# Kernel tuning notes

Measured on AMD Instinct MI355X. Metric: run time of the kernel, lower is better.

The kernel has to match this reference:

```python
import jax, jax.numpy as jnp
import numpy as np

B, S, D = 4, 2048, 512
BETA = 1.0
PARAM_SCALE = 1.0 / np.sqrt(D)  # ~ torch Linear default init scale


def setup_inputs() -> dict:
    key = jax.random.key(0)
    ks = jax.random.split(key, 14)
    def rn(k, shape, scale=1.0):
        return (jax.random.normal(k, shape, jnp.float32) * scale).astype(jnp.float32)
    return {
        "x_re": rn(ks[0], (B, S, D)),
        "x_im": rn(ks[1], (B, S, D)),
        "Wq_re": rn(ks[2], (D, D), PARAM_SCALE), "Wq_im": rn(ks[3], (D, D), PARAM_SCALE),
        "bq_re": rn(ks[4], (D,), PARAM_SCALE),   "bq_im": rn(ks[5], (D,), PARAM_SCALE),
        "Wk_re": rn(ks[6], (D, D), PARAM_SCALE), "Wk_im": rn(ks[7], (D, D), PARAM_SCALE),
        "bk_re": rn(ks[8], (D,), PARAM_SCALE),   "bk_im": rn(ks[9], (D,), PARAM_SCALE),
        "Wv_re": rn(ks[10], (D, D), PARAM_SCALE), "Wv_im": rn(ks[11], (D, D), PARAM_SCALE),
        "bv_re": rn(ks[12], (D,), PARAM_SCALE),   "bv_im": rn(ks[13], (D,), PARAM_SCALE),
    }


def reference(x_re, x_im, Wq_re, Wq_im, bq_re, bq_im,
              Wk_re, Wk_im, bk_re, bk_im, Wv_re, Wv_im, bv_re, bv_im):
    cx = lambda re, im: (re + 1j * im).astype(jnp.complex64)
    x = cx(x_re, x_im)                          # [B,S,D] complex64
    # nn.Linear: y = x @ W.T + b (complex)
    Q = jnp.einsum('bsd,ed->bse', x, cx(Wq_re, Wq_im)) + cx(bq_re, bq_im)
    K = jnp.einsum('bsd,ed->bse', x, cx(Wk_re, Wk_im)) + cx(bk_re, bk_im)
    V = jnp.einsum('bsd,ed->bse', x, cx(Wv_re, Wv_im)) + cx(bv_re, bv_im)
    # energy = -Re(Q K^H); attn = softmax(-beta * energy) = softmax(beta * Re(Q K^H))
    scores = jnp.real(jnp.einsum('bse,bte->bst', Q, jnp.conj(K)))  # [B,S,S] float32
    attn = jax.nn.softmax(BETA * scores, axis=-1)
    out = jnp.einsum('bst,bte->bse', attn.astype(jnp.complex64), V)  # [B,S,D] complex64
    return out
```

## Files before the change

### kernel.cpp

```cpp
#include <hip/hip_runtime.h>
#include <hip/hip_bf16.h>
#include <cstdint>
#include <cstddef>


typedef unsigned short u16;
typedef __attribute__((ext_vector_type(8))) _Float16 half8;
typedef __attribute__((ext_vector_type(4))) float f32x4;

#define B_    4
#define S_    2048
#define D_    512
#define M_TOT (B_ * S_)
#define KC    (2 * D_)
#define N1    (6 * D_)
#define RE_PLANE 4194304

#define X_ELEMS  ((size_t)M_TOT * KC)
#define W_ELEMS  ((size_t)N1 * KC)
#define QK_ELEMS ((size_t)M_TOT * KC)
#define VT_ELEMS ((size_t)B_ * KC * S_)
#define AT_ELEMS ((size_t)M_TOT * S_)

__device__ __forceinline__ u16 f2h(float f) {
    _Float16 h = (_Float16)f;
    return __builtin_bit_cast(u16, h);
}
__device__ __forceinline__ float h2f(u16 b) {
    return (float)__builtin_bit_cast(_Float16, b);
}

__device__ __forceinline__ f32x4 mfma16(half8 a, half8 b, f32x4 c) {
    return __builtin_amdgcn_mfma_f32_16x16x32_f16(a, b, c, 0, 0, 0);
}

__device__ __forceinline__ void dma16(const u16* g, u16* l) {
    __builtin_amdgcn_global_load_lds(
        (const __attribute__((address_space(1))) unsigned int*)g,
        (__attribute__((address_space(3))) unsigned int*)l,
        16, 0, 0);
}

__device__ __forceinline__ void stage_half(u16* __restrict__ plane,
                                           const u16* __restrict__ src,
                                           int rowbase, int kcol, int tid) {
#pragma unroll
    for (int i = 0; i < 2; ++i) {
        int c = tid + (i << 9);
        int c2 = c ^ (((c >> 5) & 1) << 1);
        int row = ((c2 >> 3) << 1) | ((c2 >> 2) & 1);
        int ks = c2 & 3;
        dma16(src + (size_t)(rowbase + row) * KC + (kcol + ks * 8),
              plane + c * 8);
    }
}

__device__ __forceinline__ void stage_half8(u16* __restrict__ plane,
                                            const u16* __restrict__ src,
                                            int ld, int rowbase, int kcol,
                                            int tid) {
#pragma unroll
    for (int i = 0; i < 2; ++i) {
        int c = tid + (i << 8);
        int c2 = c ^ (((c >> 5) & 1) << 1);
        int row = ((c2 >> 3) << 1) | ((c2 >> 2) & 1);
        int ks = c2 & 3;
        dma16(src + (size_t)(rowbase + row) * ld + (kcol + ks * 8),
              plane + c * 8);
    }
}

#define VMW(N) asm volatile("s_waitcnt vmcnt(" #N ")" ::: "memory")
#define BAR()  __builtin_amdgcn_s_barrier()

__global__ void k_diag(float* __restrict__ out, int out_size, float val) {
    int i = blockIdx.x * 256 + threadIdx.x;
    if (i < out_size && i < 4096) out[i] = val;
}

__global__ void k_prep(const float* __restrict__ xr, const float* __restrict__ xi,
                       const float* __restrict__ Wqr, const float* __restrict__ Wqi,
                       const float* __restrict__ Wkr, const float* __restrict__ Wki,
                       const float* __restrict__ Wvr, const float* __restrict__ Wvi,
                       const float* __restrict__ bqr, const float* __restrict__ bqi,
                       const float* __restrict__ bkr, const float* __restrict__ bki,
                       const float* __restrict__ bvr, const float* __restrict__ bvi,
                       u16* __restrict__ Xh, u16* __restrict__ Xl,
                       u16* __restrict__ Wh, float* __restrict__ bc) {
    int gb = blockIdx.x;
    int tid = threadIdx.x;
    if (gb < 16384) {
        int id = gb * 256 + tid;
        int m = id >> 9, d = id & 511;
        size_t o = (size_t)m * KC + d;
        if (o + D_ >= X_ELEMS) return;
        float vr = xr[id], vi = xi[id];
        u16 h;
        h = f2h(vr); Xh[o] = h;        Xl[o] = f2h(vr - h2f(h));
        h = f2h(vi); Xh[o + D_] = h;   Xl[o + D_] = f2h(vi - h2f(h));
    } else if (gb < 16384 + 12288) {
        int id = (gb - 16384) * 256 + tid;
        int n = id >> 10, k = id & 1023;
        int q = n >> 9, e = n & 511;
        int half = k >> 9, d = k & 511;
        const float* Wre = (q < 2) ? Wqr : ((q < 4) ? Wkr : Wvr);
        const float* Wim = (q < 2) ? Wqi : ((q < 4) ? Wki : Wvi);
        size_t src = (size_t)e * D_ + d;
        float v;
        if ((q & 1) == 0) v = half ? -Wim[src] : Wre[src];
        else              v = half ?  Wre[src] : Wim[src];
        if ((size_t)id < W_ELEMS) Wh[id] = f2h(v);
    } else {
        int id = (gb - 16384 - 12288) * 256 + tid;
        if (id >= N1) return;
        int q = id >> 9, e = id & 511;
        const float* src = (q == 0) ? bqr : (q == 1) ? bqi : (q == 2) ? bkr
                         : (q == 3) ? bki : (q == 4) ? bvr : bvi;
        bc[id] = src[e];
    }
}

#define RDA(d, pl, mg)                                                        \
  { const u16* _pa = &lds[pl][0];                                             \
    _Pragma("unroll")                                                         \
    for (int _i = 0; _i < 4; ++_i)                                            \
      d[_i] = *(const half8*)(_pa + aoffs + ((mg) * 4 + _i) * 512); }
#define RDB(d, pl)                                                            \
  { const u16* _pb = &lds[pl][0];                                             \
    _Pragma("unroll")                                                         \
    for (int _i = 0; _i < 4; ++_i)                                            \
      d[_i] = *(const half8*)(_pb + boffs + _i * 512); }
#define MF16(av, bv, mg)                                                      \
  { __builtin_amdgcn_s_setprio(1);                                            \
    _Pragma("unroll")                                                         \
    for (int _j = 0; _j < 4; ++_j) {                                          \
      _Pragma("unroll")                                                       \
      for (int _i = 0; _i < 4; ++_i)                                          \
        acc[(mg) * 4 + _i][_j] =                                              \
            mfma16(av[_i], bv[_j], acc[(mg) * 4 + _i][_j]);                   \
    }                                                                         \
    __builtin_amdgcn_s_setprio(0); }

#define W0(P, STG, WT) { MF16(aA, bA, 0); RDA(aB, ((P) << 2) | 0, 1); STG; WT; BAR(); }
#define W1(P, STG)     { MF16(aB, bA, 1); RDB(bB, ((P) << 2) | 3); RDA(aA, ((P) << 2) | 1, 0); STG; BAR(); }
#define W2(P, STG, WT) { MF16(aA, bB, 0); RDA(aB, ((P) << 2) | 1, 1); STG; WT; BAR(); }
#define W3(P, STG)     { MF16(aB, bB, 1); RDB(bA, (((P) ^ 1) << 2) | 2); RDA(aA, (((P) ^ 1) << 2) | 0, 0); STG; BAR(); }
#define W3L()          { MF16(aB, bB, 1); }
#define NOP_ ((void)0)

__global__ __launch_bounds__(512, 2) void k_gemm1qk(
    const u16* __restrict__ Xh, const u16* __restrict__ Xl,
    const u16* __restrict__ Wh,
    const float* __restrict__ bc,
    u16* __restrict__ Qh, u16* __restrict__ Ql,
    u16* __restrict__ Kh, u16* __restrict__ Kl) {
    __shared__ __attribute__((aligned(16))) u16 lds[8][8192];
    int tid = threadIdx.x;
    {
    }
    int L = blockIdx.y * 8 + blockIdx.x;
    int xcd = L & 7, slot = L >> 3;
    int by = xcd * 4 + (slot & 3);
    int bx = slot >> 2;
    int nb = bx * 256, mb = by * 256;
    int g = bx >> 2;
    const int NT = 32;

    int lane = tid & 63, wave = tid >> 6;
    int wm = (wave >> 2) * 128, wn = (wave & 3) * 64;
    int lr = lane & 15, lq = lane >> 4;
    int lqs8 = (lq ^ (((lr >> 3) & 1) << 1)) * 8;
    int aoffs = (wm + lr) * 32 + lqs8;
    int boffs = (wn + lr) * 32 + lqs8;

    f32x4 acc[8][4] = {};
    half8 aA[4], aB[4], bA[4], bB[4];

    stage_half(&lds[0][0], Xh, mb, 0, tid);
    stage_half(&lds[2][0], Wh, nb, 0, tid);
    stage_half(&lds[1][0], Xh, mb, 32, tid);
    stage_half(&lds[3][0], Wh, nb, 32, tid);
    stage_half(&lds[4][0], Xh, mb, 64, tid);
    stage_half(&lds[6][0], Wh, nb, 64, tid);
    VMW(8);
    BAR();
    RDB(bA, 2);
    RDA(aA, 0, 0);

    for (int t = 0; t < NT - 2; ++t) {
        const int p = t & 1;
        const u16* s1 = ((t + 1) >= 16) ? Xl : Xh;
        const int k1 = (((t + 1) & 15) << 6) + 32;
        const u16* s2 = ((t + 2) >= 16) ? Xl : Xh;
        const int k2 = ((t + 2) & 15) << 6;
        W0(p, stage_half(&lds[((p ^ 1) << 2) | 1][0], s1, mb, k1, tid), VMW(6));
        W1(p, stage_half(&lds[((p ^ 1) << 2) | 3][0], Wh, nb, k1, tid));
        W2(p, stage_half(&lds[(p << 2) | 0][0], s2, mb, k2, tid), VMW(6));
        W3(p, stage_half(&lds[(p << 2) | 2][0], Wh, nb, k2, tid));
    }
    {
        const int k1 = ((31 & 15) << 6) + 32;
        W0(0, stage_half(&lds[(1 << 2) | 1][0], Xl, mb, k1, tid), VMW(6));
        W1(0, stage_half(&lds[(1 << 2) | 3][0], Wh, nb, k1, tid));
        W2(0, NOP_, VMW(4));
        W3(0, NOP_);
    }
    {
        W0(1, NOP_, VMW(0));
        W1(1, NOP_);
        W2(1, NOP_, NOP_);
        W3L();
    }

#pragma unroll
    for (int j = 0; j < 4; ++j) {
        int n_g = nb + wn + j * 16 + lr;
        float bias = bc[n_g];
        int c = n_g & 1023;
        u16* dh = g ? Kh : Qh;
        u16* dl = g ? Kl : Ql;
#pragma unroll
        for (int i = 0; i < 8; ++i) {
            int m0 = mb + wm + i * 16 + lq * 4;
#pragma unroll
            for (int r = 0; r < 4; ++r) {
                float v = acc[i][j][r] + bias;
                u16 h = f2h(v);
                size_t idx = (size_t)(m0 + r) * KC + c;
                if (idx < QK_ELEMS) {
                    dh[idx] = h;
                    dl[idx] = f2h(v - h2f(h));
                }
            }
        }
    }
}

__global__ __launch_bounds__(256, 2) void k_gemm1v(
    const u16* __restrict__ Xh, const u16* __restrict__ Wh,
    const float* __restrict__ bc, u16* __restrict__ VT) {
    __shared__ __attribute__((aligned(16))) u16 lds[8][4096];
    int tid = threadIdx.x;
    int L = blockIdx.y * 8 + blockIdx.x;
    int xcd = L & 7, slot = L >> 3;
    int by = xcd * 8 + (slot & 7);
    int bx = slot >> 3;
    int nb = 2048 + bx * 128;
    int mb = by * 128;

    int lane = tid & 63, wave = tid >> 6;
    int wm = (wave >> 1) * 64, wn = (wave & 1) * 64;
    int lr = lane & 15, lq = lane >> 4;
    int lqs8 = (lq ^ (((lr >> 3) & 1) << 1)) * 8;
    int aoffs = (wm + lr) * 32 + lqs8;
    int boffs = (wn + lr) * 32 + lqs8;

    f32x4 acc[4][4] = {};
    half8 aA[4], aB[4], bA[4], bB[4];

    stage_half8(&lds[0][0], Xh, KC, mb, 0, tid);
    stage_half8(&lds[2][0], Wh, KC, nb, 0, tid);
    stage_half8(&lds[1][0], Xh, KC, mb, 32, tid);
    stage_half8(&lds[3][0], Wh, KC, nb, 32, tid);
    stage_half8(&lds[4][0], Xh, KC, mb, 64, tid);
    stage_half8(&lds[6][0], Wh, KC, nb, 64, tid);
    VMW(4);
    BAR();
    RDA(aA, 0, 0);
    RDB(bA, 2);

    for (int t = 0; t < 14; ++t) {
        const int p = t & 1;
        const int k1 = (t + 1) * 64 + 32;
        const int k2 = (t + 2) * 64;
        MF16(aA, bA, 0);
        RDA(aB, (p << 2) | 1, 0);
        RDB(bB, (p << 2) | 3);
        stage_half8(&lds[((p ^ 1) << 2) | 1][0], Xh, KC, mb, k1, tid);
        stage_half8(&lds[((p ^ 1) << 2) | 3][0], Wh, KC, nb, k1, tid);
        VMW(4);
        BAR();
        MF16(aB, bB, 0);
        RDA(aA, ((p ^ 1) << 2) | 0, 0);
        RDB(bA, ((p ^ 1) << 2) | 2);
        stage_half8(&lds[(p << 2) | 0][0], Xh, KC, mb, k2, tid);
        stage_half8(&lds[(p << 2) | 2][0], Wh, KC, nb, k2, tid);
        VMW(4);
        BAR();
    }
    {
        MF16(aA, bA, 0);
        RDA(aB, 1, 0);
        RDB(bB, 3);
        stage_half8(&lds[(1 << 2) | 1][0], Xh, KC, mb, 15 * 64 + 32, tid);
        stage_half8(&lds[(1 << 2) | 3][0], Wh, KC, nb, 15 * 64 + 32, tid);
        VMW(4);
        BAR();
        MF16(aB, bB, 0);
        RDA(aA, (1 << 2) | 0, 0);
        RDB(bA, (1 << 2) | 2);
        VMW(0);
        BAR();
    }
    {
        MF16(aA, bA, 0);
        RDA(aB, (1 << 2) | 1, 0);
        RDB(bB, (1 << 2) | 3);
        MF16(aB, bB, 0);
    }

#pragma unroll
    for (int j = 0; j < 4; ++j) {
        int n_g = nb + wn + j * 16 + lr;
        float bias = bc[n_g];
        int c = n_g & 1023;
#pragma unroll
        for (int i = 0; i < 4; ++i) {
            int m0 = mb + wm + i * 16 + lq * 4;
            int bidx = m0 >> 11, s0 = m0 & 2047;
            u16 pk[4];
#pragma unroll
            for (int r = 0; r < 4; ++r) pk[r] = f2h(acc[i][j][r] + bias);
            size_t idx = ((size_t)(bidx * KC + c)) * S_ + s0;
            if (idx + 3 < VT_ELEMS)
                *(ushort4*)&VT[idx] = make_ushort4(pk[0], pk[1], pk[2], pk[3]);
        }
    }
}

__global__ __launch_bounds__(512, 2) void k_gemm2_256(
    const u16* __restrict__ Qh, const u16* __restrict__ Ql,
    const u16* __restrict__ Kh, const u16* __restrict__ Kl,
    float* __restrict__ SC, int zbase) {
    __shared__ __attribute__((aligned(16))) u16 lds[8][8192];
    int tid = threadIdx.x;
    int L = blockIdx.z * 64 + blockIdx.y * 8 + blockIdx.x;
    int xcd = L & 7, slot = L >> 3;
    int zl = xcd >> 1;
    int wy = ((xcd & 1) << 2) + (slot & 3);
    int wx = slot >> 2;
    int z = zbase + zl;
    const u16* Aq = Qh + (size_t)z * S_ * KC;
    const u16* Al = Ql + (size_t)z * S_ * KC;
    const u16* Bh = Kh + (size_t)z * S_ * KC;
    const u16* Bl = Kl + (size_t)z * S_ * KC;
    int nb = wx * 256, mb = wy * 256;
    const int NT = 48;

    int lane = tid & 63, wave = tid >> 6;
    int wm = (wave >> 2) * 128, wn = (wave & 3) * 64;
    int lr = lane & 15, lq = lane >> 4;
    int lqs8 = (lq ^ (((lr >> 3) & 1) << 1)) * 8;
    int aoffs = (wm + lr) * 32 + lqs8;
    int boffs = (wn + lr) * 32 + lqs8;

    f32x4 acc[8][4] = {};
    half8 aA[4], aB[4], bA[4], bB[4];

    stage_half(&lds[0][0], Aq, mb, 0, tid);
    stage_half(&lds[2][0], Bh, nb, 0, tid);
    stage_half(&lds[1][0], Aq, mb, 32, tid);
    stage_half(&lds[3][0], Bh, nb, 32, tid);
    stage_half(&lds[4][0], Aq, mb, 64, tid);
    stage_half(&lds[6][0], Bh, nb, 64, tid);
    VMW(8);
    BAR();
    RDB(bA, 2);
    RDA(aA, 0, 0);

    for (int t = 0; t < NT - 2; ++t) {
        const int p = t & 1;
        const int t1 = t + 1, t2 = t + 2;
        const int sg1 = t1 >> 4, sg2 = t2 >> 4;
        const u16* a1 = (sg1 == 1) ? Al : Aq;
        const u16* b1 = (sg1 == 2) ? Bl : Bh;
        const u16* a2 = (sg2 == 1) ? Al : Aq;
        const u16* b2 = (sg2 == 2) ? Bl : Bh;
        const int k1 = ((t1 & 15) << 6) + 32;
        const int k2 = (t2 & 15) << 6;
        W0(p, stage_half(&lds[((p ^ 1) << 2) | 1][0], a1, mb, k1, tid), VMW(6));
        W1(p, stage_half(&lds[((p ^ 1) << 2) | 3][0], b1, nb, k1, tid));
        W2(p, stage_half(&lds[(p << 2) | 0][0], a2, mb, k2, tid), VMW(6));
        W3(p, stage_half(&lds[(p << 2) | 2][0], b2, nb, k2, tid));
    }
    {
        const int k1 = ((47 & 15) << 6) + 32;
        W0(0, stage_half(&lds[(1 << 2) | 1][0], Aq, mb, k1, tid), VMW(6));
        W1(0, stage_half(&lds[(1 << 2) | 3][0], Bl, nb, k1, tid));
        W2(0, NOP_, VMW(4));
        W3(0, NOP_);
    }
    {
        W0(1, NOP_, VMW(0));
        W1(1, NOP_);
        W2(1, NOP_, NOP_);
        W3L();
    }

    size_t sc_limit = (size_t)gridDim.z * S_ * S_;
#pragma unroll
    for (int j = 0; j < 4; ++j) {
        int n_g = nb + wn + j * 16 + lr;
#pragma unroll
        for (int i = 0; i < 8; ++i) {
            int m0 = mb + wm + i * 16 + lq * 4;
#pragma unroll
            for (int r = 0; r < 4; ++r) {
                size_t idx = ((size_t)zl * S_ + m0 + r) * S_ + n_g;
                if (idx < sc_limit) SC[idx] = acc[i][j][r];
            }
        }
    }
}

__global__ __launch_bounds__(256, 2) void k_gemm2w(
    const u16* __restrict__ Qh, const u16* __restrict__ Ql,
    const u16* __restrict__ Kh, const u16* __restrict__ Kl,
    float* __restrict__ SC, int zbase) {
    __shared__ __attribute__((aligned(16))) u16 lds[8][4096];
    int tid = threadIdx.x;
    int z = zbase + blockIdx.z;
    const u16* Aq  = Qh + (size_t)z * S_ * KC;
    const u16* Alo = Ql + (size_t)z * S_ * KC;
    const u16* Bh  = Kh + (size_t)z * S_ * KC;
    const u16* Blo = Kl + (size_t)z * S_ * KC;
    int nb = blockIdx.x * 128, mb = blockIdx.y * 128;

    int lane = tid & 63, wave = tid >> 6;
    int wm = (wave >> 1) * 64, wn = (wave & 1) * 64;
    int lr = lane & 15, lq = lane >> 4;
    int lqs8 = (lq ^ (((lr >> 3) & 1) << 1)) * 8;
    int aoffs = (wm + lr) * 32 + lqs8;
    int boffs = (wn + lr) * 32 + lqs8;

    f32x4 acc[4][4] = {};
    half8 aA[4], aB[4], bA[4], bB[4];

    stage_half8(&lds[0][0], Aq, KC, mb, 0, tid);
    stage_half8(&lds[2][0], Bh, KC, nb, 0, tid);
    stage_half8(&lds[1][0], Aq, KC, mb, 32, tid);
    stage_half8(&lds[3][0], Bh, KC, nb, 32, tid);
    stage_half8(&lds[4][0], Aq, KC, mb, 64, tid);
    stage_half8(&lds[6][0], Bh, KC, nb, 64, tid);
    VMW(4);
    BAR();
    RDA(aA, 0, 0);
    RDB(bA, 2);

    for (int t = 0; t < 46; ++t) {
        const int p = t & 1;
        const int t1 = t + 1, t2 = t + 2;
        const u16* a1 = ((t1 >> 4) == 1) ? Alo : Aq;
        const u16* b1 = ((t1 >> 4) == 2) ? Blo : Bh;
        const u16* a2 = ((t2 >> 4) == 1) ? Alo : Aq;
        const u16* b2 = ((t2 >> 4) == 2) ? Blo : Bh;
        const int k1 = ((t1 & 15) << 6) + 32;
        const int k2 = (t2 & 15) << 6;
        MF16(aA, bA, 0);
        RDA(aB, (p << 2) | 1, 0);
        RDB(bB, (p << 2) | 3);
        stage_half8(&lds[((p ^ 1) << 2) | 1][0], a1, KC, mb, k1, tid);
        stage_half8(&lds[((p ^ 1) << 2) | 3][0], b1, KC, nb, k1, tid);
        VMW(4);
        BAR();
        MF16(aB, bB, 0);
        RDA(aA, ((p ^ 1) << 2) | 0, 0);
        RDB(bA, ((p ^ 1) << 2) | 2);
        stage_half8(&lds[(p << 2) | 0][0], a2, KC, mb, k2, tid);
        stage_half8(&lds[(p << 2) | 2][0], b2, KC, nb, k2, tid);
        VMW(4);
        BAR();
    }
    {
        MF16(aA, bA, 0);
        RDA(aB, 1, 0);
        RDB(bB, 3);
        stage_half8(&lds[(1 << 2) | 1][0], Aq, KC, mb, ((47 & 15) << 6) + 32, tid);
        stage_half8(&lds[(1 << 2) | 3][0], Blo, KC, nb, ((47 & 15) << 6) + 32, tid);
        VMW(4);
        BAR();
        MF16(aB, bB, 0);
        RDA(aA, (1 << 2) | 0, 0);
        RDB(bA, (1 << 2) | 2);
        VMW(0);
        BAR();
    }
    {
        MF16(aA, bA, 0);
        RDA(aB, (1 << 2) | 1, 0);
        RDB(bB, (1 << 2) | 3);
        MF16(aB, bB, 0);
    }

    size_t sc_limit = (size_t)gridDim.z * S_ * S_;
#pragma unroll
    for (int j = 0; j < 4; ++j) {
        int n_g = nb + wn + j * 16 + lr;
#pragma unroll
        for (int i = 0; i < 4; ++i) {
            int m0 = mb + wm + i * 16 + lq * 4;
#pragma unroll
            for (int r = 0; r < 4; ++r) {
                size_t idx = ((size_t)blockIdx.z * S_ + m0 + r) * S_ + n_g;
                if (idx < sc_limit) SC[idx] = acc[i][j][r];
            }
        }
    }
}

__global__ __launch_bounds__(256) void k_softmax(const float* __restrict__ SC,
                                                 u16* __restrict__ AT, int zbase) {
    int row = blockIdx.x;
    const float* src = SC + (size_t)row * S_;
    size_t drow = (size_t)zbase * S_ + row;
    u16* dst = AT + drow * S_;
    int tid = threadIdx.x;
    float4 va = *(const float4*)(src + tid * 8);
    float4 vb = *(const float4*)(src + tid * 8 + 4);
    float v[8] = {va.x, va.y, va.z, va.w, vb.x, vb.y, vb.z, vb.w};
    float m = v[0];
#pragma unroll
    for (int i = 1; i < 8; ++i) m = fmaxf(m, v[i]);
    for (int off = 32; off > 0; off >>= 1) m = fmaxf(m, __shfl_down(m, off));
    __shared__ float redm[4], reds[4];
    if ((tid & 63) == 0) redm[tid >> 6] = m;
    __syncthreads();
    m = fmaxf(fmaxf(redm[0], redm[1]), fmaxf(redm[2], redm[3]));
    float s = 0.f;
#pragma unroll
    for (int i = 0; i < 8; ++i) { v[i] = __expf(v[i] - m); s += v[i]; }
    for (int off = 32; off > 0; off >>= 1) s += __shfl_down(s, off);
    if ((tid & 63) == 0) reds[tid >> 6] = s;
    __syncthreads();
    float inv = 1.0f / (reds[0] + reds[1] + reds[2] + reds[3]);
    if (drow * S_ + 2047 < AT_ELEMS) {
        u16 pk[8];
#pragma unroll
        for (int i = 0; i < 8; ++i) pk[i] = f2h(v[i] * inv);
        uint4 o;
        o.x = (unsigned)pk[0] | ((unsigned)pk[1] << 16);
        o.y = (unsigned)pk[2] | ((unsigned)pk[3] << 16);
        o.z = (unsigned)pk[4] | ((unsigned)pk[5] << 16);
        o.w = (unsigned)pk[6] | ((unsigned)pk[7] << 16);
        *(uint4*)(dst + tid * 8) = o;
    }
}

__global__ __launch_bounds__(256, 2) void k_gemm3w(
    const u16* __restrict__ AT, const u16* __restrict__ VT,
    float* __restrict__ out, int out_size, int full) {
    __shared__ __attribute__((aligned(16))) u16 lds[8][4096];
    int tid = threadIdx.x;
    int L = blockIdx.z * 128 + blockIdx.y * 8 + blockIdx.x;
    int xcd = L & 7, slot = L >> 3;
    int z = xcd >> 1;
    int wy = ((xcd & 1) << 3) + (slot & 7);
    int wx = slot >> 3;
    const u16* Abase = AT + (size_t)z * S_ * S_;
    const u16* Bbase = VT + (size_t)z * KC * S_;
    int nb = wx * 128, mb = wy * 128;

    int lane = tid & 63, wave = tid >> 6;
    int wm = (wave >> 1) * 64, wn = (wave & 1) * 64;
    int lr = lane & 15, lq = lane >> 4;
    int lqs8 = (lq ^ (((lr >> 3) & 1) << 1)) * 8;
    int aoffs = (wm + lr) * 32 + lqs8;
    int boffs = (wn + lr) * 32 + lqs8;

    f32x4 acc[4][4] = {};
    half8 aA[4], aB[4], bA[4], bB[4];

    stage_half8(&lds[0][0], Abase, S_, mb, 0, tid);
    stage_half8(&lds[2][0], Bbase, S_, nb, 0, tid);
    stage_half8(&lds[1][0], Abase, S_, mb, 32, tid);
    stage_half8(&lds[3][0], Bbase, S_, nb, 32, tid);
    stage_half8(&lds[4][0], Abase, S_, mb, 64, tid);
    stage_half8(&lds[6][0], Bbase, S_, nb, 64, tid);
    VMW(4);
    BAR();
    RDA(aA, 0, 0);
    RDB(bA, 2);

    for (int t = 0; t < 30; ++t) {
        const int p = t & 1;
        const int k1 = (t + 1) * 64 + 32;
        const int k2 = (t + 2) * 64;
        MF16(aA, bA, 0);
        RDA(aB, (p << 2) | 1, 0);
        RDB(bB, (p << 2) | 3);
        stage_half8(&lds[((p ^ 1) << 2) | 1][0], Abase, S_, mb, k1, tid);
        stage_half8(&lds[((p ^ 1) << 2) | 3][0], Bbase, S_, nb, k1, tid);
        VMW(4);
        BAR();
        MF16(aB, bB, 0);
        RDA(aA, ((p ^ 1) << 2) | 0, 0);
        RDB(bA, ((p ^ 1) << 2) | 2);
        stage_half8(&lds[(p << 2) | 0][0], Abase, S_, mb, k2, tid);
        stage_half8(&lds[(p << 2) | 2][0], Bbase, S_, nb, k2, tid);
        VMW(4);
        BAR();
    }
    {
        MF16(aA, bA, 0);
        RDA(aB, 1, 0);
        RDB(bB, 3);
        stage_half8(&lds[(1 << 2) | 1][0], Abase, S_, mb, 31 * 64 + 32, tid);
        stage_half8(&lds[(1 << 2) | 3][0], Bbase, S_, nb, 31 * 64 + 32, tid);
        VMW(4);
        BAR();
        MF16(aB, bB, 0);
        RDA(aA, (1 << 2) | 0, 0);
        RDB(bA, (1 << 2) | 2);
        VMW(0);
        BAR();
    }
    {
        MF16(aA, bA, 0);
        RDA(aB, (1 << 2) | 1, 0);
        RDB(bB, (1 << 2) | 3);
        MF16(aB, bB, 0);
    }

#pragma unroll
    for (int j = 0; j < 4; ++j) {
        int f = nb + wn + j * 16 + lr;
#pragma unroll
        for (int i = 0; i < 4; ++i) {
            int s0 = mb + wm + i * 16 + lq * 4;
#pragma unroll
            for (int r = 0; r < 4; ++r) {
                size_t base = ((size_t)z * S_ + s0 + r) * D_;
                if (f < D_) {
                    size_t o = base + f;
                    if (o < (size_t)out_size) out[o] = acc[i][j][r];
                } else if (full) {
                    size_t o = (size_t)RE_PLANE + base + (f - D_);
                    if (o < (size_t)out_size) out[o] = acc[i][j][r];
                }
            }
        }
    }
}


extern "C" void kernel_launch(void* const* d_in, const int* in_sizes, int n_in,
                              void* d_out, int out_size, void* d_ws, size_t ws_size,
                              hipStream_t stream) {
    (void)in_sizes; (void)n_in;
    const float* xr  = (const float*)d_in[0];
    const float* xi  = (const float*)d_in[1];
    const float* Wqr = (const float*)d_in[2];
    const float* Wqi = (const float*)d_in[3];
    const float* bqr = (const float*)d_in[4];
    const float* bqi = (const float*)d_in[5];
    const float* Wkr = (const float*)d_in[6];
    const float* Wki = (const float*)d_in[7];
    const float* bkr = (const float*)d_in[8];
    const float* bki = (const float*)d_in[9];
    const float* Wvr = (const float*)d_in[10];
    const float* Wvi = (const float*)d_in[11];
    const float* bvr = (const float*)d_in[12];
    const float* bvi = (const float*)d_in[13];
    float* out = (float*)d_out;

    constexpr size_t SZ_X  = X_ELEMS * 2;
    constexpr size_t SZ_W  = W_ELEMS * 2;
    constexpr size_t SZ_BC = (size_t)N1 * 4;
    constexpr size_t SZ_QK = QK_ELEMS * 2;
    constexpr size_t SZ_VT = VT_ELEMS * 2;
    constexpr size_t SZ_SC_B = (size_t)S_ * S_ * 4;

    char* p = (char*)d_ws;
    size_t off = 0;
    auto take = [&](size_t sz) {
        char* r = p + off;
        off += (sz + 255) & ~(size_t)255;
        return r;
    };
    u16*   Xh = (u16*)take(SZ_X);
    u16*   Xl = (u16*)take(SZ_X);
    u16*   Wh = (u16*)take(SZ_W);
    float* bc = (float*)take(SZ_BC);
    u16*   Qh = (u16*)take(SZ_QK);
    u16*   Ql = (u16*)take(SZ_QK);
    u16*   Kh = (u16*)take(SZ_QK);
    u16*   Kl = (u16*)take(SZ_QK);
    u16*   VT = (u16*)take(SZ_VT);
    u16*   AT = Xh;
    float* SC = (float*)(p + off);

    int nz = 0;
    if (ws_size > off) nz = (int)((ws_size - off) / SZ_SC_B);
    if (nz > B_) nz = B_;
    if (nz < 1) {
        k_diag<<<16, 256, 0, stream>>>(out, out_size, 1000.0f + (float)(ws_size >> 20));
        return;
    }

    int full = (out_size >= 2 * RE_PLANE) ? 1 : 0;

    k_prep<<<16384 + 12288 + 12, 256, 0, stream>>>(
        xr, xi, Wqr, Wqi, Wkr, Wki, Wvr, Wvi,
        bqr, bqi, bkr, bki, bvr, bvi, Xh, Xl, Wh, bc);
    k_gemm1qk<<<dim3(8, 32), 512, 0, stream>>>(Xh, Xl, Wh, bc, Qh, Ql, Kh, Kl);
    k_gemm1v<<<dim3(8, 64), 256, 0, stream>>>(Xh, Wh, bc, VT);

    for (int z0 = 0; z0 < B_; z0 += nz) {
        int zc = (B_ - z0 < nz) ? (B_ - z0) : nz;
        if (zc == B_) {
            k_gemm2_256<<<dim3(S_ / 256, S_ / 256, zc), 512, 0, stream>>>(
                Qh, Ql, Kh, Kl, SC, z0);
        } else {
            k_gemm2w<<<dim3(S_ / 128, S_ / 128, zc), 256, 0, stream>>>(
                Qh, Ql, Kh, Kl, SC, z0);
        }
        k_softmax<<<zc * S_, 256, 0, stream>>>(SC, AT, z0);
    }
    k_gemm3w<<<dim3(KC / 128, S_ / 128, B_), 256, 0, stream>>>(AT, VT, out, out_size, full);
}
```

Baseline: 378.9 us.

## Restructure QK^T GEMM main loop into a 4-slot LDS ring with register double-buffering

Replaces the scores GEMM's hand-scheduled 4-phase W0..W3 pipeline with a simpler 4-slot LDS ring. Each step stages a half K-tile of both A and B three steps ahead, reads fragments for the next step into alternating X/Y register sets, then issues MFMAs on the current set. The aim is one barrier per half-tile and deeper prefetch than the interleaved per-fragment schedule. The cost is more register pressure from two full fragment sets, and less intra-phase interleaving of LDS reads with MFMAs.

```diff
diff --git a/kernel.cpp b/kernel.cpp
--- a/kernel.cpp
+++ b/kernel.cpp
@@ -156,8 +156,6 @@
     u16* __restrict__ Kh, u16* __restrict__ Kl) {
     __shared__ __attribute__((aligned(16))) u16 lds[8][8192];
     int tid = threadIdx.x;
-    {
-    }
     int L = blockIdx.y * 8 + blockIdx.x;
     int xcd = L & 7, slot = L >> 3;
     int by = xcd * 4 + (slot & 3);
@@ -327,6 +325,16 @@
         }
     }
 }
+
+#define G2_SRCA(kh) ((((kh) >> 5) == 1) ? Al : Aq)
+#define G2_SRCB(kh) ((((kh) >> 5) == 2) ? Bl : Bh)
+#define G2_KC(kh)   ((((((kh) >> 1)) & 15) << 6) + (((kh) & 1) << 5))
+#define G2_STG(kh)                                                            \
+  { stage_half(&lds[(kh) & 3][0], G2_SRCA(kh), mb, G2_KC(kh), tid);           \
+    stage_half(&lds[4 + ((kh) & 3)][0], G2_SRCB(kh), nb, G2_KC(kh), tid); }
+#define G2_RD(S, kh)                                                          \
+  { RDA(a0##S, (kh) & 3, 0); RDA(a1##S, (kh) & 3, 1); RDB(b##S, 4 + ((kh) & 3)); }
+#define G2_MF(S) { MF16(a0##S, b##S, 0); MF16(a1##S, b##S, 1); }
 
 __global__ __launch_bounds__(512, 2) void k_gemm2_256(
     const u16* __restrict__ Qh, const u16* __restrict__ Ql,
@@ -345,7 +353,6 @@
     const u16* Bh = Kh + (size_t)z * S_ * KC;
     const u16* Bl = Kl + (size_t)z * S_ * KC;
     int nb = wx * 256, mb = wy * 256;
-    const int NT = 48;
 
     int lane = tid & 63, wave = tid >> 6;
     int wm = (wave >> 2) * 128, wn = (wave & 3) * 64;
@@ -355,47 +362,24 @@
     int boffs = (wn + lr) * 32 + lqs8;
 
     f32x4 acc[8][4] = {};
-    half8 aA[4], aB[4], bA[4], bB[4];
-
-    stage_half(&lds[0][0], Aq, mb, 0, tid);
-    stage_half(&lds[2][0], Bh, nb, 0, tid);
-    stage_half(&lds[1][0], Aq, mb, 32, tid);
-    stage_half(&lds[3][0], Bh, nb, 32, tid);
-    stage_half(&lds[4][0], Aq, mb, 64, tid);
-    stage_half(&lds[6][0], Bh, nb, 64, tid);
-    VMW(8);
+    half8 a0X[4], a1X[4], bX[4];
+    half8 a0Y[4], a1Y[4], bY[4];
+
+    G2_STG(0);
+    G2_STG(1);
+    G2_STG(2);
+    VMW(4);
     BAR();
-    RDB(bA, 2);
-    RDA(aA, 0, 0);
-
-    for (int t = 0; t < NT - 2; ++t) {
-        const int p = t & 1;
-        const int t1 = t + 1, t2 = t + 2;
-        const int sg1 = t1 >> 4, sg2 = t2 >> 4;
-        const u16* a1 = (sg1 == 1) ? Al : Aq;
-        const u16* b1 = (sg1 == 2) ? Bl : Bh;
-        const u16* a2 = (sg2 == 1) ? Al : Aq;
-        const u16* b2 = (sg2 == 2) ? Bl : Bh;
-        const int k1 = ((t1 & 15) << 6) + 32;
-        const int k2 = (t2 & 15) << 6;
-        W0(p, stage_half(&lds[((p ^ 1) << 2) | 1][0], a1, mb, k1, tid), VMW(6));
-        W1(p, stage_half(&lds[((p ^ 1) << 2) | 3][0], b1, nb, k1, tid));
-        W2(p, stage_half(&lds[(p << 2) | 0][0], a2, mb, k2, tid), VMW(6));
-        W3(p, stage_half(&lds[(p << 2) | 2][0], b2, nb, k2, tid));
-    }
-    {
-        const int k1 = ((47 & 15) << 6) + 32;
-        W0(0, stage_half(&lds[(1 << 2) | 1][0], Aq, mb, k1, tid), VMW(6));
-        W1(0, stage_half(&lds[(1 << 2) | 3][0], Bl, nb, k1, tid));
-        W2(0, NOP_, VMW(4));
-        W3(0, NOP_);
-    }
-    {
-        W0(1, NOP_, VMW(0));
-        W1(1, NOP_);
-        W2(1, NOP_, NOP_);
-        W3L();
-    }
+    G2_RD(Y, 0);
+
+    for (int w = 0; w < 92; w += 2) {
+        G2_RD(X, w + 1); G2_MF(Y); G2_STG(w + 3); VMW(4); BAR();
+        G2_RD(Y, w + 2); G2_MF(X); G2_STG(w + 4); VMW(4); BAR();
+    }
+    G2_RD(X, 93); G2_MF(Y); G2_STG(95); VMW(4); BAR();
+    G2_RD(Y, 94); G2_MF(X); VMW(0); BAR();
+    G2_RD(X, 95); G2_MF(Y);
+    G2_MF(X);
 
     size_t sc_limit = (size_t)gridDim.z * S_ * S_;
 #pragma unroll
@@ -708,7 +692,7 @@
     for (int z0 = 0; z0 < B_; z0 += nz) {
         int zc = (B_ - z0 < nz) ? (B_ - z0) : nz;
         if (zc == B_) {
-            k_gemm2_256<<<dim3(S_ / 256, S_ / 256, zc), 512, 0, stream>>>(
+            k_gemm2_256<<<dim3(8, 8, 4), 512, 0, stream>>>(
                 Qh, Ql, Kh, Kl, SC, z0);
         } else {
             k_gemm2w<<<dim3(S_ / 128, S_ / 128, zc), 256, 0, stream>>>(
```

Result: no change. 381.3 us (+0.6%).
